# Kernel tuning notes

Hardware: AMD Instinct MI355X
Metric: run time of the kernel (lower is better)

## Reference

```python
import jax, jax.numpy as jnp
import numpy as np

N, D, F, C = 50000, 32, 128, 16
LN_EPS = 1e-5
CLAMP_MIN = 1e-5


def _layernorm_1d(x):
    # LayerNorm over the full node vector, no affine (elementwise_affine=False)
    m = x.mean()
    v = x.var()  # biased, matches torch LayerNorm
    return (x - m) / jnp.sqrt(v + LN_EPS)


def setup_inputs() -> dict:
    key = jax.random.key(0)
    k1, k2, k3, k4, k5, k6 = jax.random.split(key, 6)
    return {
        "h": jax.random.normal(k1, (N, F), dtype=jnp.float32),
        "logits": jax.random.normal(k2, (N, C), dtype=jnp.float32),
        "old_z": jax.random.uniform(k3, (N,), dtype=jnp.float32),
        "tau_1": jax.random.uniform(k4, (1,), dtype=jnp.float32),
        "tau_2": jax.random.uniform(k5, (1,), dtype=jnp.float32),
        "nbr": jax.random.randint(k6, (N, D), 0, N, dtype=jnp.int32),
    }


def reference(h, logits, old_z, tau_1, tau_2, nbr):
    # --- mailbox pass 1: neighbor logits -> adaptive gating features ---
    pred = jnp.argmax(logits[nbr], axis=2)          # [N, D] neighbor class preds
    center_pred = jnp.argmax(logits, axis=1)        # [N]
    # n_degree = 1 in the source (counts, not fractions) -- reproduced faithfully
    f1 = jnp.sum(pred == center_pred[:, None], axis=1).astype(h.dtype)  # [N]
    cnts = jax.nn.one_hot(pred, C, dtype=h.dtype).sum(axis=1)           # [N, C]
    cnts_p = jnp.clip(cnts, CLAMP_MIN, None)
    f2 = -jnp.sum(cnts_p * jnp.log(cnts_p), axis=1)                     # [N]
    f1 = jax.lax.stop_gradient(f1)
    f2 = jax.lax.stop_gradient(f2)

    norm_f1 = _layernorm_1d(f1)
    norm_f2 = _layernorm_1d(f2)
    # shared_tau=True path: tau_1, tau_2 passed in ([1] broadcasts over [N])
    z = jax.nn.sigmoid(-(norm_f1 - tau_1)) * jax.nn.sigmoid(-(norm_f2 - tau_2))  # [N]
    gate = jnp.minimum(old_z, z)

    # --- mailbox pass 2: scatter-sum of neighbor features ---
    agg = h[nbr].sum(axis=1)                        # [N, F]
    normagg = jax.nn.relu(agg)
    new_h = h + gate[:, None] * normagg
    return new_h, z
```

## Files before the change

kernel.cpp:

```cpp
#include <hip/hip_runtime.h>
#include <math.h>

#define NN 50000
#define DEG 32
#define FDIM 128
#define NCLS 16
#define LN_EPS 1e-5f
#define CLAMP_MIN 1e-5f

#define PRED_NB 196
#define CONV_NB 512
#define NGROUPS (NN * FDIM / 8)
#define FEAT_NB 196

#define SLICES 4
#define SL_U32 (NN * 16)
#define AGG_BPS ((NN * 4 + 255) / 256)
#define AGG_NB (SLICES * AGG_BPS)

typedef float  nf4 __attribute__((ext_vector_type(4)));
typedef unsigned nu4 __attribute__((ext_vector_type(4)));
typedef int    ni4 __attribute__((ext_vector_type(4)));

__device__ inline unsigned bf_rne(float x) {
    unsigned u = __float_as_uint(x);
    u += 0x7fffu + ((u >> 16) & 1u);
    return u >> 16;
}

__global__ __launch_bounds__(256) void k_pre(const float* __restrict__ logits,
                                             unsigned char* __restrict__ pred8,
                                             const float* __restrict__ h,
                                             unsigned* __restrict__ hb,
                                             unsigned* __restrict__ zs) {
    int b = blockIdx.x;
    if (b < PRED_NB) {
        if (b == 0 && threadIdx.x < 5) zs[threadIdx.x] = 0u;
        int i = b * 256 + threadIdx.x;
        if (i >= NN) return;
        const nf4* lp = (const nf4*)(logits + (long)i * NCLS);
        float best = -INFINITY;
        int bi = 0;
#pragma unroll
        for (int q = 0; q < 4; ++q) {
            nf4 v = __builtin_nontemporal_load(lp + q);
#pragma unroll
            for (int r = 0; r < 4; ++r) {
                if (v[r] > best) { best = v[r]; bi = q * 4 + r; }
            }
        }
        pred8[i] = (unsigned char)bi;
    } else {
        int g0 = (b - PRED_NB) * 256 + threadIdx.x;
        for (int g = g0; g < NGROUPS; g += CONV_NB * 256) {
            const nf4* src = (const nf4*)(h + (long)g * 8);
            nf4 a = __builtin_nontemporal_load(src);
            nf4 c = __builtin_nontemporal_load(src + 1);
            nu4 o;
            o.x = bf_rne(a.x) | (bf_rne(a.y) << 16);
            o.y = bf_rne(a.z) | (bf_rne(a.w) << 16);
            o.z = bf_rne(c.x) | (bf_rne(c.y) << 16);
            o.w = bf_rne(c.z) | (bf_rne(c.w) << 16);
            int node = g >> 4;
            int q    = (g >> 2) & 3;
            int sub  = g & 3;
            ((nu4*)hb)[(size_t)q * (NN * 4) + node * 4 + sub] = o;
        }
    }
}

__global__ __launch_bounds__(256) void k_feats_lds(const int* __restrict__ nbr,
                                                   const unsigned char* __restrict__ pred8,
                                                   float* __restrict__ f1,
                                                   float* __restrict__ f2,
                                                   float* __restrict__ acc4,
                                                   unsigned* __restrict__ ctr,
                                                   float* __restrict__ params, int n) {
    __shared__ unsigned char lp[NN];
    {
        const uint4* s4 = (const uint4*)pred8;
        uint4* d4 = (uint4*)lp;
        for (int i = threadIdx.x; i < 3125; i += 256) d4[i] = s4[i];
    }
    __syncthreads();
    int node = blockIdx.x * 256 + threadIdx.x;
    float v1 = 0.f, v2 = 0.f;
    if (node < n) {
        unsigned long long lo = 0ull, hi = 0ull;
        const ni4* np = (const ni4*)(nbr + (long)node * DEG);
#pragma unroll
        for (int q = 0; q < 8; ++q) {
            ni4 k4 = __builtin_nontemporal_load(np + q);
            int ks[4] = {k4.x, k4.y, k4.z, k4.w};
#pragma unroll
            for (int r = 0; r < 4; ++r) {
                int p = lp[ks[r]];
                unsigned long long inc = 1ull << ((p & 7) * 8);
                if (p < 8) lo += inc; else hi += inc;
            }
        }
        int cp = lp[node];
        unsigned long long src = (cp < 8) ? lo : hi;
        v1 = (float)((src >> ((cp & 7) * 8)) & 0xffull);
        float ent = 0.f;
#pragma unroll
        for (int c = 0; c < NCLS; ++c) {
            unsigned long long s = (c < 8) ? lo : hi;
            float cnt = (float)((s >> ((c & 7) * 8)) & 0xffull);
            float x = fmaxf(cnt, CLAMP_MIN);
            ent -= x * __logf(x);
        }
        v2 = ent;
        f1[node] = v1;
        f2[node] = v2;
    }
    float s0 = v1, s1 = v1 * v1, s2 = v2, s3 = v2 * v2;
#pragma unroll
    for (int off = 32; off > 0; off >>= 1) {
        s0 += __shfl_down(s0, off);
        s1 += __shfl_down(s1, off);
        s2 += __shfl_down(s2, off);
        s3 += __shfl_down(s3, off);
    }
    __shared__ float red[4][4];
    int wid = threadIdx.x >> 6;
    if ((threadIdx.x & 63) == 0) {
        red[wid][0] = s0; red[wid][1] = s1; red[wid][2] = s2; red[wid][3] = s3;
    }
    __syncthreads();
    if (threadIdx.x == 0) {
        float t0 = 0.f, t1 = 0.f, t2 = 0.f, t3 = 0.f;
#pragma unroll
        for (int w = 0; w < 4; ++w) {
            t0 += red[w][0]; t1 += red[w][1]; t2 += red[w][2]; t3 += red[w][3];
        }
        atomicAdd(&acc4[0], t0);
        atomicAdd(&acc4[1], t1);
        atomicAdd(&acc4[2], t2);
        atomicAdd(&acc4[3], t3);
        __threadfence();
        unsigned old = atomicAdd(ctr, 1u);
        if (old == FEAT_NB - 1) {
            double u0 = (double)atomicAdd(&acc4[0], 0.f);
            double u1 = (double)atomicAdd(&acc4[1], 0.f);
            double u2 = (double)atomicAdd(&acc4[2], 0.f);
            double u3 = (double)atomicAdd(&acc4[3], 0.f);
            double inv_n = 1.0 / (double)NN;
            double m1 = u0 * inv_n;
            double var1 = u1 * inv_n - m1 * m1;
            double m2 = u2 * inv_n;
            double var2 = u3 * inv_n - m2 * m2;
            params[0] = (float)m1;
            params[1] = (float)(1.0 / sqrt(var1 + (double)LN_EPS));
            params[2] = (float)m2;
            params[3] = (float)(1.0 / sqrt(var2 + (double)LN_EPS));
        }
    }
}

#define U2F(x) __uint_as_float(x)

#define ISSUE(buf, base) do {                                                   \
    buf[0] = ((const nu4*)(slab + (size_t)kk[(base) + 0] * 16))[lane];          \
    buf[1] = ((const nu4*)(slab + (size_t)kk[(base) + 1] * 16))[lane];          \
    buf[2] = ((const nu4*)(slab + (size_t)kk[(base) + 2] * 16))[lane];          \
    buf[3] = ((const nu4*)(slab + (size_t)kk[(base) + 3] * 16))[lane];          \
} while (0)

#define CONSUME(buf) do {                                                       \
    _Pragma("unroll")                                                           \
    for (int s2 = 0; s2 < 4; ++s2) {                                            \
        acc[0] += U2F(buf[s2].x << 16); acc[1] += U2F(buf[s2].x & 0xffff0000u); \
        acc[2] += U2F(buf[s2].y << 16); acc[3] += U2F(buf[s2].y & 0xffff0000u); \
        acc[4] += U2F(buf[s2].z << 16); acc[5] += U2F(buf[s2].z & 0xffff0000u); \
        acc[6] += U2F(buf[s2].w << 16); acc[7] += U2F(buf[s2].w & 0xffff0000u); \
    }                                                                           \
} while (0)

__global__ __launch_bounds__(256) void k_agg_sl(const unsigned* __restrict__ hb,
                                                const int* __restrict__ nbr,
                                                const float* __restrict__ old_z,
                                                const float* __restrict__ tau1,
                                                const float* __restrict__ tau2,
                                                const float* __restrict__ f1,
                                                const float* __restrict__ f2,
                                                const float* __restrict__ params,
                                                float* __restrict__ out_h,
                                                float* __restrict__ out_z, int n) {
    int q = blockIdx.x / AGG_BPS;
    int t = (blockIdx.x - q * AGG_BPS) * 256 + threadIdx.x;
    int node = t >> 2;
    int lane = t & 3;
    if (node >= n) return;
    const unsigned* slab = hb + (size_t)q * SL_U32;

    const ni4* np = (const ni4*)(nbr + (long)node * DEG);
    int kk[32];
#pragma unroll
    for (int j = 0; j < 8; ++j) {
        ni4 v = np[j];
        kk[4 * j + 0] = v.x; kk[4 * j + 1] = v.y;
        kk[4 * j + 2] = v.z; kk[4 * j + 3] = v.w;
    }

    float acc[8];
#pragma unroll
    for (int i = 0; i < 8; ++i) acc[i] = 0.f;

    nu4 A[4], B[4];
    ISSUE(A, 0);  ISSUE(B, 4);
    CONSUME(A);   ISSUE(A, 8);
    CONSUME(B);   ISSUE(B, 12);
    CONSUME(A);   ISSUE(A, 16);
    CONSUME(B);   ISSUE(B, 20);
    CONSUME(A);   ISSUE(A, 24);
    CONSUME(B);   ISSUE(B, 28);
    CONSUME(A);   CONSUME(B);

    float a = (f1[node] - params[0]) * params[1] - tau1[0];
    float b = (f2[node] - params[2]) * params[3] - tau2[0];
    float z = 1.f / ((1.f + expf(a)) * (1.f + expf(b)));
    float gate = fminf(old_z[node], z);

    nu4 hid = ((const nu4*)(slab + (size_t)node * 16))[lane];
    nf4 o0, o1;
    o0.x = U2F(hid.x << 16)          + gate * fmaxf(acc[0], 0.f);
    o0.y = U2F(hid.x & 0xffff0000u)  + gate * fmaxf(acc[1], 0.f);
    o0.z = U2F(hid.y << 16)          + gate * fmaxf(acc[2], 0.f);
    o0.w = U2F(hid.y & 0xffff0000u)  + gate * fmaxf(acc[3], 0.f);
    o1.x = U2F(hid.z << 16)          + gate * fmaxf(acc[4], 0.f);
    o1.y = U2F(hid.z & 0xffff0000u)  + gate * fmaxf(acc[5], 0.f);
    o1.z = U2F(hid.w << 16)          + gate * fmaxf(acc[6], 0.f);
    o1.w = U2F(hid.w & 0xffff0000u)  + gate * fmaxf(acc[7], 0.f);
    nf4* op = (nf4*)(out_h + (long)node * FDIM + q * 32 + lane * 8);
    __builtin_nontemporal_store(o0, op);
    __builtin_nontemporal_store(o1, op + 1);
    if (q == 0 && lane == 0) __builtin_nontemporal_store(z, out_z + node);
}

extern "C" void kernel_launch(void* const* d_in, const int* in_sizes, int n_in,
                              void* d_out, int out_size, void* d_ws, size_t ws_size,
                              hipStream_t stream) {
    const float* h      = (const float*)d_in[0];
    const float* logits = (const float*)d_in[1];
    const float* old_z  = (const float*)d_in[2];
    const float* tau1   = (const float*)d_in[3];
    const float* tau2   = (const float*)d_in[4];
    const int*   nbr    = (const int*)d_in[5];

    char* ws = (char*)d_ws;
    float*         params   = (float*)ws;
    float*         acc4     = (float*)(ws + 16);
    unsigned*      ctr      = (unsigned*)(ws + 32);
    unsigned char* pred8    = (unsigned char*)(ws + 32768);
    float*         f1       = (float*)(ws + 90112);
    float*         f2       = (float*)(ws + 294912);
    unsigned*      hb       = (unsigned*)(ws + 524288);

    float* out_h = (float*)d_out;
    float* out_z = out_h + (long)NN * FDIM;

    k_pre      <<<PRED_NB + CONV_NB, 256, 0, stream>>>(logits, pred8, h, hb, (unsigned*)(ws + 16));
    k_feats_lds<<<FEAT_NB, 256, 0, stream>>>(nbr, pred8, f1, f2, acc4, ctr, params, NN);
    k_agg_sl   <<<AGG_NB, 256, 0, stream>>>(hb, nbr, old_z, tau1, tau2,
                                            f1, f2, params, out_h, out_z, NN);
}
```

Before: 158.1 us.

## Fuse three kernels into one cooperative persistent kernel with grid syncs

Replaces the pre-pass, feature, and aggregation kernels with a single cooperative kernel that uses grid-wide syncs between phases, removing two launch boundaries. The feature phase drops the per-block LDS copy of all class predictions and reads pred8 from global memory instead. It splits each node's neighbour counting across four threads combined with shuffles. The fixed grid size assumes 256 CUs, and the three grid.sync barriers plus the loss of LDS caching may cost more than the launch overhead they remove.

```diff
diff --git a/kernel.cpp b/kernel.cpp
--- a/kernel.cpp
+++ b/kernel.cpp
@@ -1,5 +1,8 @@
 #include <hip/hip_runtime.h>
+#include <hip/hip_cooperative_groups.h>
 #include <math.h>
+
+namespace cg = cooperative_groups;
 
 #define NN 50000
 #define DEG 32
@@ -7,16 +10,10 @@
 #define NCLS 16
 #define LN_EPS 1e-5f
 #define CLAMP_MIN 1e-5f
-
-#define PRED_NB 196
-#define CONV_NB 512
 #define NGROUPS (NN * FDIM / 8)
-#define FEAT_NB 196
-
 #define SLICES 4
 #define SL_U32 (NN * 16)
-#define AGG_BPS ((NN * 4 + 255) / 256)
-#define AGG_NB (SLICES * AGG_BPS)
+#define AGG_W ((long)SLICES * NN * 4)
 
 typedef float  nf4 __attribute__((ext_vector_type(4)));
 typedef unsigned nu4 __attribute__((ext_vector_type(4)));
@@ -26,136 +23,6 @@
     unsigned u = __float_as_uint(x);
     u += 0x7fffu + ((u >> 16) & 1u);
     return u >> 16;
-}
-
-__global__ __launch_bounds__(256) void k_pre(const float* __restrict__ logits,
-                                             unsigned char* __restrict__ pred8,
-                                             const float* __restrict__ h,
-                                             unsigned* __restrict__ hb,
-                                             unsigned* __restrict__ zs) {
-    int b = blockIdx.x;
-    if (b < PRED_NB) {
-        if (b == 0 && threadIdx.x < 5) zs[threadIdx.x] = 0u;
-        int i = b * 256 + threadIdx.x;
-        if (i >= NN) return;
-        const nf4* lp = (const nf4*)(logits + (long)i * NCLS);
-        float best = -INFINITY;
-        int bi = 0;
-#pragma unroll
-        for (int q = 0; q < 4; ++q) {
-            nf4 v = __builtin_nontemporal_load(lp + q);
-#pragma unroll
-            for (int r = 0; r < 4; ++r) {
-                if (v[r] > best) { best = v[r]; bi = q * 4 + r; }
-            }
-        }
-        pred8[i] = (unsigned char)bi;
-    } else {
-        int g0 = (b - PRED_NB) * 256 + threadIdx.x;
-        for (int g = g0; g < NGROUPS; g += CONV_NB * 256) {
-            const nf4* src = (const nf4*)(h + (long)g * 8);
-            nf4 a = __builtin_nontemporal_load(src);
-            nf4 c = __builtin_nontemporal_load(src + 1);
-            nu4 o;
-            o.x = bf_rne(a.x) | (bf_rne(a.y) << 16);
-            o.y = bf_rne(a.z) | (bf_rne(a.w) << 16);
-            o.z = bf_rne(c.x) | (bf_rne(c.y) << 16);
-            o.w = bf_rne(c.z) | (bf_rne(c.w) << 16);
-            int node = g >> 4;
-            int q    = (g >> 2) & 3;
-            int sub  = g & 3;
-            ((nu4*)hb)[(size_t)q * (NN * 4) + node * 4 + sub] = o;
-        }
-    }
-}
-
-__global__ __launch_bounds__(256) void k_feats_lds(const int* __restrict__ nbr,
-                                                   const unsigned char* __restrict__ pred8,
-                                                   float* __restrict__ f1,
-                                                   float* __restrict__ f2,
-                                                   float* __restrict__ acc4,
-                                                   unsigned* __restrict__ ctr,
-                                                   float* __restrict__ params, int n) {
-    __shared__ unsigned char lp[NN];
-    {
-        const uint4* s4 = (const uint4*)pred8;
-        uint4* d4 = (uint4*)lp;
-        for (int i = threadIdx.x; i < 3125; i += 256) d4[i] = s4[i];
-    }
-    __syncthreads();
-    int node = blockIdx.x * 256 + threadIdx.x;
-    float v1 = 0.f, v2 = 0.f;
-    if (node < n) {
-        unsigned long long lo = 0ull, hi = 0ull;
-        const ni4* np = (const ni4*)(nbr + (long)node * DEG);
-#pragma unroll
-        for (int q = 0; q < 8; ++q) {
-            ni4 k4 = __builtin_nontemporal_load(np + q);
-            int ks[4] = {k4.x, k4.y, k4.z, k4.w};
-#pragma unroll
-            for (int r = 0; r < 4; ++r) {
-                int p = lp[ks[r]];
-                unsigned long long inc = 1ull << ((p & 7) * 8);
-                if (p < 8) lo += inc; else hi += inc;
-            }
-        }
-        int cp = lp[node];
-        unsigned long long src = (cp < 8) ? lo : hi;
-        v1 = (float)((src >> ((cp & 7) * 8)) & 0xffull);
-        float ent = 0.f;
-#pragma unroll
-        for (int c = 0; c < NCLS; ++c) {
-            unsigned long long s = (c < 8) ? lo : hi;
-            float cnt = (float)((s >> ((c & 7) * 8)) & 0xffull);
-            float x = fmaxf(cnt, CLAMP_MIN);
-            ent -= x * __logf(x);
-        }
-        v2 = ent;
-        f1[node] = v1;
-        f2[node] = v2;
-    }
-    float s0 = v1, s1 = v1 * v1, s2 = v2, s3 = v2 * v2;
-#pragma unroll
-    for (int off = 32; off > 0; off >>= 1) {
-        s0 += __shfl_down(s0, off);
-        s1 += __shfl_down(s1, off);
-        s2 += __shfl_down(s2, off);
-        s3 += __shfl_down(s3, off);
-    }
-    __shared__ float red[4][4];
-    int wid = threadIdx.x >> 6;
-    if ((threadIdx.x & 63) == 0) {
-        red[wid][0] = s0; red[wid][1] = s1; red[wid][2] = s2; red[wid][3] = s3;
-    }
-    __syncthreads();
-    if (threadIdx.x == 0) {
-        float t0 = 0.f, t1 = 0.f, t2 = 0.f, t3 = 0.f;
-#pragma unroll
-        for (int w = 0; w < 4; ++w) {
-            t0 += red[w][0]; t1 += red[w][1]; t2 += red[w][2]; t3 += red[w][3];
-        }
-        atomicAdd(&acc4[0], t0);
-        atomicAdd(&acc4[1], t1);
-        atomicAdd(&acc4[2], t2);
-        atomicAdd(&acc4[3], t3);
-        __threadfence();
-        unsigned old = atomicAdd(ctr, 1u);
-        if (old == FEAT_NB - 1) {
-            double u0 = (double)atomicAdd(&acc4[0], 0.f);
-            double u1 = (double)atomicAdd(&acc4[1], 0.f);
-            double u2 = (double)atomicAdd(&acc4[2], 0.f);
-            double u3 = (double)atomicAdd(&acc4[3], 0.f);
-            double inv_n = 1.0 / (double)NN;
-            double m1 = u0 * inv_n;
-            double var1 = u1 * inv_n - m1 * m1;
-            double m2 = u2 * inv_n;
-            double var2 = u3 * inv_n - m2 * m2;
-            params[0] = (float)m1;
-            params[1] = (float)(1.0 / sqrt(var1 + (double)LN_EPS));
-            params[2] = (float)m2;
-            params[3] = (float)(1.0 / sqrt(var2 + (double)LN_EPS));
-        }
-    }
 }
 
 #define U2F(x) __uint_as_float(x)
@@ -177,65 +44,181 @@
     }                                                                           \
 } while (0)
 
-__global__ __launch_bounds__(256) void k_agg_sl(const unsigned* __restrict__ hb,
-                                                const int* __restrict__ nbr,
-                                                const float* __restrict__ old_z,
-                                                const float* __restrict__ tau1,
-                                                const float* __restrict__ tau2,
-                                                const float* __restrict__ f1,
-                                                const float* __restrict__ f2,
-                                                const float* __restrict__ params,
-                                                float* __restrict__ out_h,
-                                                float* __restrict__ out_z, int n) {
-    int q = blockIdx.x / AGG_BPS;
-    int t = (blockIdx.x - q * AGG_BPS) * 256 + threadIdx.x;
-    int node = t >> 2;
-    int lane = t & 3;
-    if (node >= n) return;
-    const unsigned* slab = hb + (size_t)q * SL_U32;
-
-    const ni4* np = (const ni4*)(nbr + (long)node * DEG);
-    int kk[32];
-#pragma unroll
-    for (int j = 0; j < 8; ++j) {
-        ni4 v = np[j];
-        kk[4 * j + 0] = v.x; kk[4 * j + 1] = v.y;
-        kk[4 * j + 2] = v.z; kk[4 * j + 3] = v.w;
-    }
-
-    float acc[8];
-#pragma unroll
-    for (int i = 0; i < 8; ++i) acc[i] = 0.f;
-
-    nu4 A[4], B[4];
-    ISSUE(A, 0);  ISSUE(B, 4);
-    CONSUME(A);   ISSUE(A, 8);
-    CONSUME(B);   ISSUE(B, 12);
-    CONSUME(A);   ISSUE(A, 16);
-    CONSUME(B);   ISSUE(B, 20);
-    CONSUME(A);   ISSUE(A, 24);
-    CONSUME(B);   ISSUE(B, 28);
-    CONSUME(A);   CONSUME(B);
-
-    float a = (f1[node] - params[0]) * params[1] - tau1[0];
-    float b = (f2[node] - params[2]) * params[3] - tau2[0];
-    float z = 1.f / ((1.f + expf(a)) * (1.f + expf(b)));
-    float gate = fminf(old_z[node], z);
-
-    nu4 hid = ((const nu4*)(slab + (size_t)node * 16))[lane];
-    nf4 o0, o1;
-    o0.x = U2F(hid.x << 16)          + gate * fmaxf(acc[0], 0.f);
-    o0.y = U2F(hid.x & 0xffff0000u)  + gate * fmaxf(acc[1], 0.f);
-    o0.z = U2F(hid.y << 16)          + gate * fmaxf(acc[2], 0.f);
-    o0.w = U2F(hid.y & 0xffff0000u)  + gate * fmaxf(acc[3], 0.f);
-    o1.x = U2F(hid.z << 16)          + gate * fmaxf(acc[4], 0.f);
-    o1.y = U2F(hid.z & 0xffff0000u)  + gate * fmaxf(acc[5], 0.f);
-    o1.z = U2F(hid.w << 16)          + gate * fmaxf(acc[6], 0.f);
-    o1.w = U2F(hid.w & 0xffff0000u)  + gate * fmaxf(acc[7], 0.f);
-    nf4* op = (nf4*)(out_h + (long)node * FDIM + q * 32 + lane * 8);
-    __builtin_nontemporal_store(o0, op);
-    __builtin_nontemporal_store(o1, op + 1);
-    if (q == 0 && lane == 0) __builtin_nontemporal_store(z, out_z + node);
+__global__ __launch_bounds__(256, 4) void k_fused(
+    const float* __restrict__ logits, const float* __restrict__ h,
+    const int* __restrict__ nbr, const float* __restrict__ old_z,
+    const float* __restrict__ tau1, const float* __restrict__ tau2,
+    unsigned char* __restrict__ pred8, unsigned* __restrict__ hb,
+    float* __restrict__ f1, float* __restrict__ f2,
+    float* __restrict__ acc4, float* __restrict__ params,
+    float* __restrict__ out_h, float* __restrict__ out_z)
+{
+    cg::grid_group grid = cg::this_grid();
+    const long TT  = (long)gridDim.x * 256;
+    const long tid = (long)blockIdx.x * 256 + threadIdx.x;
+
+    if (tid < 4) acc4[tid] = 0.f;
+    for (long i = tid; i < NN; i += TT) {
+        const nf4* lp = (const nf4*)(logits + i * NCLS);
+        float best = -INFINITY;
+        int bi = 0;
+#pragma unroll
+        for (int q = 0; q < 4; ++q) {
+            nf4 v = __builtin_nontemporal_load(lp + q);
+#pragma unroll
+            for (int r = 0; r < 4; ++r) {
+                if (v[r] > best) { best = v[r]; bi = q * 4 + r; }
+            }
+        }
+        pred8[i] = (unsigned char)bi;
+    }
+    for (long g = tid; g < NGROUPS; g += TT) {
+        const nf4* src = (const nf4*)(h + g * 8);
+        nf4 a = __builtin_nontemporal_load(src);
+        nf4 c = __builtin_nontemporal_load(src + 1);
+        nu4 o;
+        o.x = bf_rne(a.x) | (bf_rne(a.y) << 16);
+        o.y = bf_rne(a.z) | (bf_rne(a.w) << 16);
+        o.z = bf_rne(c.x) | (bf_rne(c.y) << 16);
+        o.w = bf_rne(c.z) | (bf_rne(c.w) << 16);
+        int node = (int)(g >> 4);
+        int q    = (int)((g >> 2) & 3);
+        int sub  = (int)(g & 3);
+        ((nu4*)hb)[(size_t)q * (NN * 4) + (size_t)node * 4 + sub] = o;
+    }
+    grid.sync();
+
+    float bs0 = 0.f, bs1 = 0.f, bs2 = 0.f, bs3 = 0.f;
+    for (long t2 = tid; t2 < (long)NN * 4; t2 += TT) {
+        long nodeW = t2 >> 2;
+        int  part  = (int)(t2 & 3);
+        unsigned long long lo = 0ull, hi = 0ull;
+        {
+            const ni4* np = (const ni4*)(nbr + nodeW * DEG) + part * 2;
+#pragma unroll
+            for (int q = 0; q < 2; ++q) {
+                ni4 k4 = np[q];
+                int ks[4] = {k4.x, k4.y, k4.z, k4.w};
+#pragma unroll
+                for (int r = 0; r < 4; ++r) {
+                    int p = pred8[ks[r]];
+                    unsigned long long inc = 1ull << ((p & 7) * 8);
+                    if (p < 8) lo += inc; else hi += inc;
+                }
+            }
+        }
+        lo += __shfl_xor(lo, 1); lo += __shfl_xor(lo, 2);
+        hi += __shfl_xor(hi, 1); hi += __shfl_xor(hi, 2);
+        if (part == 0) {
+            int cp = pred8[nodeW];
+            unsigned long long src = (cp < 8) ? lo : hi;
+            float v1 = (float)((src >> ((cp & 7) * 8)) & 0xffull);
+            float ent = 0.f;
+#pragma unroll
+            for (int c = 0; c < NCLS; ++c) {
+                unsigned long long s = (c < 8) ? lo : hi;
+                float cnt = (float)((s >> ((c & 7) * 8)) & 0xffull);
+                float x = fmaxf(cnt, CLAMP_MIN);
+                ent -= x * __logf(x);
+            }
+            f1[nodeW] = v1;
+            f2[nodeW] = ent;
+            bs0 += v1; bs1 += v1 * v1; bs2 += ent; bs3 += ent * ent;
+        }
+    }
+#pragma unroll
+    for (int off = 32; off > 0; off >>= 1) {
+        bs0 += __shfl_down(bs0, off);
+        bs1 += __shfl_down(bs1, off);
+        bs2 += __shfl_down(bs2, off);
+        bs3 += __shfl_down(bs3, off);
+    }
+    __shared__ float red[4][4];
+    {
+        int wid = threadIdx.x >> 6;
+        if ((threadIdx.x & 63) == 0) {
+            red[wid][0] = bs0; red[wid][1] = bs1; red[wid][2] = bs2; red[wid][3] = bs3;
+        }
+        __syncthreads();
+        if (threadIdx.x == 0 && (long)blockIdx.x * 256 < (long)NN * 4) {
+            float t0 = 0.f, t1 = 0.f, t2 = 0.f, t3 = 0.f;
+#pragma unroll
+            for (int w = 0; w < 4; ++w) {
+                t0 += red[w][0]; t1 += red[w][1]; t2 += red[w][2]; t3 += red[w][3];
+            }
+            atomicAdd(&acc4[0], t0);
+            atomicAdd(&acc4[1], t1);
+            atomicAdd(&acc4[2], t2);
+            atomicAdd(&acc4[3], t3);
+        }
+    }
+    grid.sync();
+    if (tid == 0) {
+        double u0 = (double)acc4[0], u1 = (double)acc4[1];
+        double u2 = (double)acc4[2], u3 = (double)acc4[3];
+        double inv_n = 1.0 / (double)NN;
+        double m1 = u0 * inv_n;
+        double var1 = u1 * inv_n - m1 * m1;
+        double m2 = u2 * inv_n;
+        double var2 = u3 * inv_n - m2 * m2;
+        params[0] = (float)m1;
+        params[1] = (float)(1.0 / sqrt(var1 + (double)LN_EPS));
+        params[2] = (float)m2;
+        params[3] = (float)(1.0 / sqrt(var2 + (double)LN_EPS));
+    }
+    grid.sync();
+
+    const float p0 = params[0], p1 = params[1], p2 = params[2], p3 = params[3];
+    const float t1v = tau1[0], t2v = tau2[0];
+    for (long w = tid; w < AGG_W; w += TT) {
+        int  q    = (int)(w / (NN * 4));
+        long rr   = w - (long)q * (NN * 4);
+        int  node = (int)(rr >> 2);
+        int  lane = (int)(rr & 3);
+        const unsigned* slab = hb + (size_t)q * SL_U32;
+
+        const ni4* np = (const ni4*)(nbr + (long)node * DEG);
+        int kk[32];
+#pragma unroll
+        for (int j = 0; j < 8; ++j) {
+            ni4 v = np[j];
+            kk[4 * j + 0] = v.x; kk[4 * j + 1] = v.y;
+            kk[4 * j + 2] = v.z; kk[4 * j + 3] = v.w;
+        }
+        float acc[8];
+#pragma unroll
+        for (int i = 0; i < 8; ++i) acc[i] = 0.f;
+
+        nu4 A[4], B[4];
+        ISSUE(A, 0);  ISSUE(B, 4);
+        CONSUME(A);   ISSUE(A, 8);
+        CONSUME(B);   ISSUE(B, 12);
+        CONSUME(A);   ISSUE(A, 16);
+        CONSUME(B);   ISSUE(B, 20);
+        CONSUME(A);   ISSUE(A, 24);
+        CONSUME(B);   ISSUE(B, 28);
+        CONSUME(A);   CONSUME(B);
+
+        float a = (f1[node] - p0) * p1 - t1v;
+        float b = (f2[node] - p2) * p3 - t2v;
+        float z = 1.f / ((1.f + expf(a)) * (1.f + expf(b)));
+        float gate = fminf(old_z[node], z);
+
+        nu4 hid = ((const nu4*)(slab + (size_t)node * 16))[lane];
+        nf4 o0, o1;
+        o0.x = U2F(hid.x << 16)          + gate * fmaxf(acc[0], 0.f);
+        o0.y = U2F(hid.x & 0xffff0000u)  + gate * fmaxf(acc[1], 0.f);
+        o0.z = U2F(hid.y << 16)          + gate * fmaxf(acc[2], 0.f);
+        o0.w = U2F(hid.y & 0xffff0000u)  + gate * fmaxf(acc[3], 0.f);
+        o1.x = U2F(hid.z << 16)          + gate * fmaxf(acc[4], 0.f);
+        o1.y = U2F(hid.z & 0xffff0000u)  + gate * fmaxf(acc[5], 0.f);
+        o1.z = U2F(hid.w << 16)          + gate * fmaxf(acc[6], 0.f);
+        o1.w = U2F(hid.w & 0xffff0000u)  + gate * fmaxf(acc[7], 0.f);
+        nf4* op = (nf4*)(out_h + (long)node * FDIM + q * 32 + lane * 8);
+        __builtin_nontemporal_store(o0, op);
+        __builtin_nontemporal_store(o1, op + 1);
+        if (q == 0 && lane == 0) __builtin_nontemporal_store(z, out_z + node);
+    }
 }
 
 extern "C" void kernel_launch(void* const* d_in, const int* in_sizes, int n_in,
@@ -249,19 +232,27 @@
     const int*   nbr    = (const int*)d_in[5];
 
     char* ws = (char*)d_ws;
-    float*         params   = (float*)ws;
-    float*         acc4     = (float*)(ws + 16);
-    unsigned*      ctr      = (unsigned*)(ws + 32);
-    unsigned char* pred8    = (unsigned char*)(ws + 32768);
-    float*         f1       = (float*)(ws + 90112);
-    float*         f2       = (float*)(ws + 294912);
-    unsigned*      hb       = (unsigned*)(ws + 524288);
+    float*         params = (float*)ws;
+    float*         acc4   = (float*)(ws + 16);
+    unsigned char* pred8  = (unsigned char*)(ws + 32768);
+    float*         f1     = (float*)(ws + 90112);
+    float*         f2     = (float*)(ws + 294912);
+    unsigned*      hb     = (unsigned*)(ws + 524288);
 
     float* out_h = (float*)d_out;
     float* out_z = out_h + (long)NN * FDIM;
 
-    k_pre      <<<PRED_NB + CONV_NB, 256, 0, stream>>>(logits, pred8, h, hb, (unsigned*)(ws + 16));
-    k_feats_lds<<<FEAT_NB, 256, 0, stream>>>(nbr, pred8, f1, f2, acc4, ctr, params, NN);
-    k_agg_sl   <<<AGG_NB, 256, 0, stream>>>(hb, nbr, old_z, tau1, tau2,
-                                            f1, f2, params, out_h, out_z, NN);
+    static int G = 0;
+    if (G == 0) {
+        int maxb = 0;
+        if (hipOccupancyMaxActiveBlocksPerMultiprocessor(&maxb, k_fused, 256, 0) != hipSuccess
+            || maxb < 1) maxb = 4;
+        if (maxb > 8) maxb = 8;
+        G = maxb * 256;
+    }
+    void* args[] = {(void*)&logits, (void*)&h, (void*)&nbr, (void*)&old_z,
+                    (void*)&tau1, (void*)&tau2, (void*)&pred8, (void*)&hb,
+                    (void*)&f1, (void*)&f2, (void*)&acc4, (void*)&params,
+                    (void*)&out_h, (void*)&out_z};
+    hipLaunchCooperativeKernel(k_fused, dim3(G), dim3(256), args, 0, stream);
 }
```

Result: slower. 347.1 us (+119.5%).
